# Performance work log

Measured on AMD Instinct MI355X. Metric: run time of the kernel, lower is better.

Reference implementation:

```python
import jax, jax.numpy as jnp
import numpy as np
import math

B, S, D, H = 8, 512, 2048, 16
HD = D // H
TIME_INCLUDE = True
QREL_INCLUDE = True


def setup_inputs() -> dict:
    root = jax.random.key(0)
    ks = jax.random.split(root, 14)
    f32 = jnp.float32
    scale = 1.0 / math.sqrt(D)
    query = jax.random.normal(ks[0], (B, S, D), dtype=f32)
    key = jax.random.normal(ks[1], (B, S, D), dtype=f32)
    value = jax.random.normal(ks[2], (B, S, D), dtype=f32)
    rel = jax.random.uniform(ks[3], (B, S, S), dtype=f32)  # relation scores, positive
    timestamp = jax.random.uniform(ks[4], (B, S, S), dtype=f32) * 10.0  # time deltas
    # causal mask: True = masked (future positions); guarantees each row has >=1 unmasked entry
    mask = jnp.broadcast_to(jnp.triu(jnp.ones((S, S), dtype=bool), k=1), (B, S, S))
    l1 = jnp.full((1,), 0.3, dtype=f32)
    l2 = jnp.full((1,), 0.5, dtype=f32)
    pos_key_embeds = jax.random.normal(ks[5], (S, HD), dtype=f32)
    pos_value_embeds = jax.random.normal(ks[6], (S, HD), dtype=f32)
    Wq = jax.random.normal(ks[7], (D, D), dtype=f32) * scale
    bq = jnp.zeros((D,), dtype=f32)
    Wk = jax.random.normal(ks[8], (D, D), dtype=f32) * scale
    bk = jnp.zeros((D,), dtype=f32)
    Wv = jax.random.normal(ks[9], (D, D), dtype=f32) * scale
    bv = jnp.zeros((D,), dtype=f32)
    return dict(query=query, key=key, value=value, rel=rel, l1=l1, l2=l2,
                timestamp=timestamp, pos_key_embeds=pos_key_embeds,
                pos_value_embeds=pos_value_embeds, mask=mask,
                Wq=Wq, bq=bq, Wk=Wk, bk=bk, Wv=Wv, bv=bv)


def reference(query, key, value, rel, l1, l2, timestamp, pos_key_embeds, pos_value_embeds, mask, Wq, bq, Wk, bk, Wv, bv):
    b, s, d = query.shape
    l1 = l1.reshape(())
    l2 = l2.reshape(())
    # QKV projections -> [B, H, S, HD]
    q = (query @ Wq.T + bq).reshape(b, s, H, HD).transpose(0, 2, 1, 3)
    k = (key @ Wk.T + bk).reshape(b, s, H, HD).transpose(0, 2, 1, 3)
    v = (value @ Wv.T + bv).reshape(b, s, H, HD).transpose(0, 2, 1, 3)
    m = mask[:, None]  # [B,1,S,S] bool, broadcast over heads (== repeat in torch)
    # relation-score softmax: rel * mask, zeros -> -10000
    relm = rel[:, None] * m.astype(jnp.float32)
    rel_attn = jax.nn.softmax(jnp.where(relm == 0, jnp.float32(-10000.0), relm), axis=-1)
    # content scores
    scores = jnp.einsum('bhqd,bhkd->bhqk', q, k) / math.sqrt(HD)
    scores = jnp.where(m, jnp.float32(-1e9), scores)
    # time-decay scores
    ts = jnp.exp(-jnp.abs(timestamp[:, None]))
    ts = jnp.where(m, -jnp.inf, ts)
    prob_attn = jax.nn.softmax(scores, axis=-1)
    time_attn = jax.nn.softmax(ts, axis=-1)
    if TIME_INCLUDE:
        prob_attn = (1.0 - l2) * prob_attn + l2 * time_attn
    if QREL_INCLUDE:
        prob_attn = (1.0 - l1) * prob_attn + l1 * rel_attn
    if not TIME_INCLUDE:
        prob_attn = l2 * prob_attn
    out = jnp.einsum('bhqk,bhkd->bhqd', prob_attn, v)
    out = out.transpose(0, 2, 1, 3).reshape(b, s, d)
    return out, prob_attn
```

## Files before the change

kernel.cpp:

```cpp
#include <hip/hip_runtime.h>
#include <hip/hip_bf16.h>

typedef __bf16 bf16_t;
typedef __bf16 bf16x8 __attribute__((ext_vector_type(8)));
typedef float  f32x4  __attribute__((ext_vector_type(4)));

constexpr int cB = 8, cS = 512, cD = 2048, cH = 16, cHD = 128;
constexpr int cBS = cB * cS;
constexpr float kInvSqrtHD = 0.08838834764831845f;

__device__ __forceinline__ bf16x8 cvt8(float4 a, float4 b) {
    bf16x8 r;
    r[0]=(bf16_t)a.x; r[1]=(bf16_t)a.y; r[2]=(bf16_t)a.z; r[3]=(bf16_t)a.w;
    r[4]=(bf16_t)b.x; r[5]=(bf16_t)b.y; r[6]=(bf16_t)b.z; r[7]=(bf16_t)b.w;
    return r;
}

__device__ __forceinline__ void gload16(const bf16_t* g, bf16_t* l) {
    __builtin_amdgcn_global_load_lds(
        (const __attribute__((address_space(1))) void*)g,
        (__attribute__((address_space(3))) void*)l,
        16, 0, 0);
}

__device__ __forceinline__ unsigned packbf(float a, float b) {
    const unsigned short ua = __builtin_bit_cast(unsigned short, (bf16_t)a);
    const unsigned short ub = __builtin_bit_cast(unsigned short, (bf16_t)b);
    return (unsigned)ua | ((unsigned)ub << 16);
}
__device__ __forceinline__ float unpk_lo(unsigned u) {
    return (float)__builtin_bit_cast(bf16_t, (unsigned short)(u & 0xffffu));
}
__device__ __forceinline__ float unpk_hi(unsigned u) {
    return (float)__builtin_bit_cast(bf16_t, (unsigned short)(u >> 16));
}

__global__ __launch_bounds__(256) void prep_kernel(
    const float* __restrict__ q, const float* __restrict__ k, const float* __restrict__ v,
    const float* __restrict__ wq, const float* __restrict__ wk, const float* __restrict__ wv,
    const float* __restrict__ rel, const float* __restrict__ tsp,
    bf16_t* __restrict__ abf, bf16_t* __restrict__ wbf,
    bf16_t* __restrict__ t_attn, bf16_t* __restrict__ r_attn)
{
    const int y = blockIdx.y;
    if (y < 6) {
        const float* src; bf16_t* dst; size_t n8;
        if (y < 3) { src = (y==0 ? q : y==1 ? k : v);   dst = abf + (size_t)y*cBS*cD;     n8 = (size_t)cBS*cD/8; }
        else       { src = (y==3 ? wq : y==4 ? wk : wv); dst = wbf + (size_t)(y-3)*cD*cD; n8 = (size_t)cD*cD/8; }
        const size_t stride = (size_t)gridDim.x * blockDim.x;
        for (size_t idx = (size_t)blockIdx.x * blockDim.x + threadIdx.x; idx < n8; idx += stride) {
            const float4 f0 = ((const float4*)src)[2*idx];
            const float4 f1 = ((const float4*)src)[2*idx+1];
            ((bf16x8*)dst)[idx] = cvt8(f0, f1);
        }
        return;
    }
    const int lane = threadIdx.x & 63;
    const int wid  = threadIdx.x >> 6;
    const int row  = blockIdx.x * 4 + wid;
    const int i = row & 511;
    const size_t base = (size_t)row * cS;

    float vt[8], vr[8];
    #pragma unroll
    for (int u = 0; u < 8; ++u) {
        const int j = lane + 64*u;
        const float tv = tsp[base + j];
        const float rv = rel[base + j];
        vt[u] = (j <= i) ? expf(-fabsf(tv)) : -__builtin_inff();
        vr[u] = (j > i && rv != 0.0f) ? rv : -10000.0f;
    }
    float Mt = vt[0], Mr = vr[0];
    #pragma unroll
    for (int u = 1; u < 8; ++u) { Mt = fmaxf(Mt, vt[u]); Mr = fmaxf(Mr, vr[u]); }
    #pragma unroll
    for (int msk = 1; msk < 64; msk <<= 1) {
        Mt = fmaxf(Mt, __shfl_xor(Mt, msk));
        Mr = fmaxf(Mr, __shfl_xor(Mr, msk));
    }
    float St = 0.f, Sr = 0.f;
    #pragma unroll
    for (int u = 0; u < 8; ++u) {
        vt[u] = expf(vt[u] - Mt);
        vr[u] = expf(vr[u] - Mr);
        St += vt[u]; Sr += vr[u];
    }
    #pragma unroll
    for (int msk = 1; msk < 64; msk <<= 1) { St += __shfl_xor(St, msk); Sr += __shfl_xor(Sr, msk); }
    const float rSt = 1.f / St, rSr = 1.f / Sr;
    #pragma unroll
    for (int u = 0; u < 8; ++u) {
        const int j = lane + 64*u;
        t_attn[base + j] = (bf16_t)(vt[u] * rSt);
        r_attn[base + j] = (bf16_t)(vr[u] * rSr);
    }
}

__global__ __launch_bounds__(256) void proj_kernel(
    const bf16_t* __restrict__ abf, const bf16_t* __restrict__ wbf,
    const float* __restrict__ bq, const float* __restrict__ bk, const float* __restrict__ bv,
    bf16_t* __restrict__ qh, bf16_t* __restrict__ kh, bf16_t* __restrict__ vtr)
{
    const int which = blockIdx.y;
    const bf16_t* A = abf + (size_t)which * cBS * cD;
    const bf16_t* W = wbf + (size_t)which * cD * cD;
    const float* bias = (which == 0) ? bq : (which == 1) ? bk : bv;

    const int bm = blockIdx.x & 31;
    const int bn = blockIdx.x >> 5;
    const int M0 = bm << 7, N0 = bn << 7;

    __shared__ bf16_t As[3][128 * 32];
    __shared__ bf16_t Ws[3][128 * 32];

    const int tid = threadIdx.x;
    const int lane = tid & 63, wid = tid >> 6;
    const int wm = wid & 1, wn = wid >> 1;
    const int i15 = lane & 15, g = lane >> 4;

    const int srow = tid >> 2;
    const int sg   = (tid & 3) ^ (srow & 3);
    const bf16_t* aSrc = A + (size_t)(M0 + srow) * cD + sg * 8;
    const bf16_t* wSrc = W + (size_t)(N0 + srow) * cD + sg * 8;
    const size_t rowStep = (size_t)64 * cD;

    auto stage = [&](int b, int kt) {
        const int kb = kt * 32;
        gload16(aSrc + kb,           &As[b][tid * 8]);
        gload16(aSrc + kb + rowStep, &As[b][tid * 8 + 2048]);
        gload16(wSrc + kb,           &Ws[b][tid * 8]);
        gload16(wSrc + kb + rowStep, &Ws[b][tid * 8 + 2048]);
    };

    int offA[4], offW[4];
    #pragma unroll
    for (int m = 0; m < 4; ++m) {
        const int r = wm*64 + m*16 + i15;
        offA[m] = r*32 + ((g ^ (r & 3)) << 3);
    }
    #pragma unroll
    for (int n = 0; n < 4; ++n) {
        const int r = wn*64 + n*16 + i15;
        offW[n] = r*32 + ((g ^ (r & 3)) << 3);
    }

    const f32x4 zero4 = {0.f, 0.f, 0.f, 0.f};
    f32x4 acc[4][4];
    #pragma unroll
    for (int m = 0; m < 4; ++m)
        #pragma unroll
        for (int n = 0; n < 4; ++n) acc[m][n] = zero4;

    stage(0, 0);
    stage(1, 1);

    for (int kt = 0; kt < cD / 32; ++kt) {
        if (kt + 2 < cD / 32) {
            stage((kt + 2) % 3, kt + 2);
            asm volatile("s_waitcnt vmcnt(8)" ::: "memory");
        } else if (kt + 1 < cD / 32) {
            asm volatile("s_waitcnt vmcnt(4)" ::: "memory");
        } else {
            asm volatile("s_waitcnt vmcnt(0)" ::: "memory");
        }
        __builtin_amdgcn_s_barrier();
        __builtin_amdgcn_sched_barrier(0);

        const bf16_t* Ab = &As[kt % 3][0];
        const bf16_t* Wb = &Ws[kt % 3][0];
        bf16x8 a[4];
        #pragma unroll
        for (int m = 0; m < 4; ++m) a[m] = *(const bf16x8*)(Ab + offA[m]);
        #pragma unroll
        for (int n = 0; n < 4; ++n) {
            const bf16x8 w = *(const bf16x8*)(Wb + offW[n]);
            #pragma unroll
            for (int m = 0; m < 4; ++m)
                acc[m][n] = __builtin_amdgcn_mfma_f32_16x16x32_bf16(a[m], w, acc[m][n], 0, 0, 0);
        }
        __builtin_amdgcn_s_barrier();
    }

    #pragma unroll
    for (int n = 0; n < 4; ++n) {
        const int col = N0 + wn*64 + n*16 + i15;
        const float bb = bias[col];
        const int hh = col >> 7, hd = col & 127;
        #pragma unroll
        for (int m = 0; m < 4; ++m) {
            const int rowl = wm*64 + m*16 + (g << 2);
            #pragma unroll
            for (int r = 0; r < 4; ++r) {
                const int R = M0 + rowl + r;
                const int bbi = R >> 9, ss = R & 511;
                const float val = acc[m][n][r] + bb;
                if (which == 2)
                    vtr[((size_t)(bbi*cH + hh) * cHD + hd) * cS + ss] = (bf16_t)val;
                else if (which == 0)
                    qh[((size_t)(bbi*cH + hh) * cS + ss) * cHD + hd] = (bf16_t)val;
                else
                    kh[((size_t)(bbi*cH + hh) * cS + ss) * cHD + hd] = (bf16_t)val;
            }
        }
    }
}

__global__ __launch_bounds__(256) void attn_kernel(
    const bf16_t* __restrict__ qh, const bf16_t* __restrict__ kh,
    const bf16_t* __restrict__ vtr,
    const bf16_t* __restrict__ t_attn, const bf16_t* __restrict__ r_attn,
    const float* __restrict__ l1p, const float* __restrict__ l2p,
    float* __restrict__ probOut, float* __restrict__ out)
{
    const int itile = blockIdx.x & 7;
    const int bh = blockIdx.x >> 3;
    const int b = bh >> 4, h = bh & 15;
    const int i0 = itile * 64;

    const float l1 = l1p[0], l2 = l2p[0];
    const float ap = (1.f - l1) * (1.f - l2);
    const float at = (1.f - l1) * l2;
    const float ar = l1;

    __shared__ bf16_t qps[64][136];
    __shared__ bf16_t ks[64][136];
    __shared__ bf16_t vs[2][128 * 64];

    const int tid = threadIdx.x, lane = tid & 63, wid = tid >> 6;
    const int i15 = lane & 15, g = lane >> 4;

    {
        const int row = tid >> 2, d0 = (tid & 3) << 5;
        const bf16_t* src = qh + ((size_t)bh * cS + i0 + row) * cHD + d0;
        #pragma unroll
        for (int q = 0; q < 4; ++q)
            *(bf16x8*)(&qps[row][d0 + q*8]) = *(const bf16x8*)(src + q*8);
    }
    __syncthreads();
    bf16x8 aq[4];
    #pragma unroll
    for (int kk = 0; kk < 4; ++kk)
        aq[kk] = *(const bf16x8*)(&qps[wid*16 + i15][kk*32 + (g << 3)]);

    const int iBase = i0 + wid*16 + (g << 2);

    auto stageK = [&](int kt) {
        const int row = tid >> 2, d0 = (tid & 3) << 5;
        const bf16_t* src = kh + ((size_t)bh * cS + kt*64 + row) * cHD + d0;
        #pragma unroll
        for (int q = 0; q < 4; ++q)
            *(bf16x8*)(&ks[row][d0 + q*8]) = *(const bf16x8*)(src + q*8);
    };
    auto stageVissue = [&](int kt, int buf) {
        #pragma unroll
        for (int e4 = 0; e4 < 4; ++e4) {
            const int e = e4 * 256 + tid;
            const int hd = e >> 3, j8 = e & 7;
            const int jsw = (j8 ^ (hd & 7)) << 3;
            gload16(vtr + ((size_t)bh * cHD + hd) * cS + kt*64 + jsw, &vs[buf][e * 8]);
        }
    };

    float srow[4] = {0.f, 0.f, 0.f, 0.f};
    unsigned es[8][8];
    #pragma unroll
    for (int kt = 0; kt < 8; ++kt) {
        if (kt <= itile) {
            __syncthreads();
            stageK(kt);
            __syncthreads();
            f32x4 acc[4];
            const f32x4 zero4 = {0.f, 0.f, 0.f, 0.f};
            #pragma unroll
            for (int n = 0; n < 4; ++n) acc[n] = zero4;
            #pragma unroll
            for (int kk = 0; kk < 4; ++kk)
                #pragma unroll
                for (int n = 0; n < 4; ++n) {
                    bf16x8 bk = *(const bf16x8*)(&ks[n*16 + i15][kk*32 + (g << 3)]);
                    acc[n] = __builtin_amdgcn_mfma_f32_16x16x32_bf16(aq[kk], bk, acc[n], 0, 0, 0);
                }
            #pragma unroll
            for (int n = 0; n < 4; ++n) {
                const int j = kt*64 + n*16 + i15;
                float e[4];
                #pragma unroll
                for (int r = 0; r < 4; ++r) {
                    const int i = iBase + r;
                    e[r] = (j > i) ? 0.f : __expf(acc[n][r] * kInvSqrtHD);
                    srow[r] += e[r];
                }
                es[kt][n*2]     = packbf(e[0], e[1]);
                es[kt][n*2 + 1] = packbf(e[2], e[3]);
            }
        }
    }
    float rs[4];
    #pragma unroll
    for (int r = 0; r < 4; ++r) {
        float s = srow[r];
        #pragma unroll
        for (int msk = 1; msk < 16; msk <<= 1) s += __shfl_xor(s, msk);
        rs[r] = 1.f / s;
    }

    f32x4 oacc[8];
    const f32x4 zero4o = {0.f, 0.f, 0.f, 0.f};
    #pragma unroll
    for (int n2 = 0; n2 < 8; ++n2) oacc[n2] = zero4o;

    stageVissue(0, 0);

    #pragma unroll
    for (int kt = 0; kt < 8; ++kt) {
        const bool hasP = (kt <= itile);
        #pragma unroll
        for (int n = 0; n < 4; ++n) {
            float e[4] = {0.f, 0.f, 0.f, 0.f};
            if (hasP) {
                const unsigned p0 = es[kt][n*2], p1 = es[kt][n*2 + 1];
                e[0] = unpk_lo(p0); e[1] = unpk_hi(p0);
                e[2] = unpk_lo(p1); e[3] = unpk_hi(p1);
            }
            const int j = kt*64 + n*16 + i15;
            #pragma unroll
            for (int r = 0; r < 4; ++r) {
                const int i = iBase + r;
                const float p = e[r] * rs[r];
                const size_t tri = (size_t)(b*cS + i) * cS + j;
                const float tv = (float)t_attn[tri];
                const float rv = (float)r_attn[tri];
                const float mixed = ap*p + at*tv + ar*rv;
                probOut[((size_t)bh * cS + i) * cS + j] = mixed;
                qps[wid*16 + (g << 2) + r][n*16 + i15] = (bf16_t)mixed;
            }
        }
        asm volatile("s_waitcnt lgkmcnt(0)" ::: "memory");
        __builtin_amdgcn_sched_barrier(0);
        asm volatile("s_waitcnt vmcnt(16)" ::: "memory");
        __builtin_amdgcn_s_barrier();
        #pragma unroll
        for (int kk = 0; kk < 2; ++kk) {
            const bf16x8 pa = *(const bf16x8*)(&qps[wid*16 + i15][kk*32 + (g << 3)]);
            #pragma unroll
            for (int n2 = 0; n2 < 8; ++n2) {
                const int hd = n2*16 + i15;
                const int jb = (kk*64 + g*16) ^ ((hd & 7) << 4);
                const bf16x8 bvv = *(const bf16x8*)((const char*)&vs[kt & 1][0] + hd*128 + jb);
                oacc[n2] = __builtin_amdgcn_mfma_f32_16x16x32_bf16(pa, bvv, oacc[n2], 0, 0, 0);
            }
        }
        if (kt < 7) stageVissue(kt + 1, (kt + 1) & 1);
    }

    #pragma unroll
    for (int n2 = 0; n2 < 8; ++n2) {
        const int hd = n2*16 + i15;
        #pragma unroll
        for (int r = 0; r < 4; ++r) {
            const int i = i0 + wid*16 + (g << 2) + r;
            out[(size_t)(b*cS + i) * cD + h*cHD + hd] = oacc[n2][r];
        }
    }
}

extern "C" void kernel_launch(void* const* d_in, const int* in_sizes, int n_in,
                              void* d_out, int out_size, void* d_ws, size_t ws_size,
                              hipStream_t stream)
{
    const float* query = (const float*)d_in[0];
    const float* keyi  = (const float*)d_in[1];
    const float* value = (const float*)d_in[2];
    const float* rel   = (const float*)d_in[3];
    const float* l1    = (const float*)d_in[4];
    const float* l2    = (const float*)d_in[5];
    const float* tsp   = (const float*)d_in[6];
    const float* Wq    = (const float*)d_in[10];
    const float* bq    = (const float*)d_in[11];
    const float* Wk    = (const float*)d_in[12];
    const float* bk    = (const float*)d_in[13];
    const float* Wv    = (const float*)d_in[14];
    const float* bv    = (const float*)d_in[15];

    char* ws = (char*)d_ws;
    const size_t projBytes = (size_t)cB * cH * cS * cHD * 2;
    bf16_t* qh  = (bf16_t*)(ws);
    bf16_t* kh  = (bf16_t*)(ws + projBytes);
    bf16_t* vtr = (bf16_t*)(ws + 2 * projBytes);
    const size_t trBytes = (size_t)cB * cS * cS * 2;
    bf16_t* tat = (bf16_t*)(ws + 3 * projBytes);
    bf16_t* rat = (bf16_t*)(ws + 3 * projBytes + trBytes);

    float* out = (float*)d_out;
    float* probOut = out + (size_t)cB * cS * cD;

    bf16_t* abf = (bf16_t*)probOut;
    bf16_t* wbf = abf + (size_t)3 * cBS * cD;

    prep_kernel<<<dim3(1024, 7), 256, 0, stream>>>(query, keyi, value, Wq, Wk, Wv,
                                                   rel, tsp, abf, wbf, tat, rat);
    proj_kernel<<<dim3(512, 3), 256, 0, stream>>>(abf, wbf, bq, bk, bv, qh, kh, vtr);
    attn_kernel<<<cB * cH * (cS / 64), 256, 0, stream>>>(qh, kh, vtr, tat, rat, l1, l2, probOut, out);
}
```

Before: 262.1 us.

## Replace triple-buffered K=32 projection pipeline with single-buffer K=64 tiles

The QKV projection GEMM loop drops the three-stage LDS ring (K=32 per stage, manual vmcnt waits) for a single LDS buffer holding a K=64 tile, with the XOR swizzle widened to 8 chunks. Each iteration loads the tile, synchronizes, and runs two 32-wide MFMA sub-steps. The aim is fewer barriers per unit of K and a smaller LDS footprint (32KB instead of 48KB), which could let more blocks share a CU. The cost is that global loads no longer overlap with MFMA work inside a block, so latency hiding depends on other resident blocks.

```diff
diff --git a/kernel.cpp b/kernel.cpp
--- a/kernel.cpp
+++ b/kernel.cpp
@@ -110,38 +110,34 @@
     const int bn = blockIdx.x >> 5;
     const int M0 = bm << 7, N0 = bn << 7;
 
-    __shared__ bf16_t As[3][128 * 32];
-    __shared__ bf16_t Ws[3][128 * 32];
+    __shared__ bf16_t As[128 * 64];
+    __shared__ bf16_t Ws[128 * 64];
 
     const int tid = threadIdx.x;
     const int lane = tid & 63, wid = tid >> 6;
     const int wm = wid & 1, wn = wid >> 1;
     const int i15 = lane & 15, g = lane >> 4;
 
-    const int srow = tid >> 2;
-    const int sg   = (tid & 3) ^ (srow & 3);
-    const bf16_t* aSrc = A + (size_t)(M0 + srow) * cD + sg * 8;
-    const bf16_t* wSrc = W + (size_t)(N0 + srow) * cD + sg * 8;
-    const size_t rowStep = (size_t)64 * cD;
-
-    auto stage = [&](int b, int kt) {
-        const int kb = kt * 32;
-        gload16(aSrc + kb,           &As[b][tid * 8]);
-        gload16(aSrc + kb + rowStep, &As[b][tid * 8 + 2048]);
-        gload16(wSrc + kb,           &Ws[b][tid * 8]);
-        gload16(wSrc + kb + rowStep, &Ws[b][tid * 8 + 2048]);
-    };
+    const int sr0 = tid >> 3;
+    const int sgc = ((tid & 7) ^ (sr0 & 7)) << 3;
+    const bf16_t* aSrc[4];
+    const bf16_t* wSrc[4];
+    #pragma unroll
+    for (int l = 0; l < 4; ++l) {
+        aSrc[l] = A + (size_t)(M0 + l*32 + sr0) * cD + sgc;
+        wSrc[l] = W + (size_t)(N0 + l*32 + sr0) * cD + sgc;
+    }
 
     int offA[4], offW[4];
     #pragma unroll
     for (int m = 0; m < 4; ++m) {
         const int r = wm*64 + m*16 + i15;
-        offA[m] = r*32 + ((g ^ (r & 3)) << 3);
+        offA[m] = r*64 + ((g ^ (r & 7)) << 3);
     }
     #pragma unroll
     for (int n = 0; n < 4; ++n) {
         const int r = wn*64 + n*16 + i15;
-        offW[n] = r*32 + ((g ^ (r & 3)) << 3);
+        offW[n] = r*64 + ((g ^ (r & 7)) << 3);
     }
 
     const f32x4 zero4 = {0.f, 0.f, 0.f, 0.f};
@@ -151,34 +147,29 @@
         #pragma unroll
         for (int n = 0; n < 4; ++n) acc[m][n] = zero4;
 
-    stage(0, 0);
-    stage(1, 1);
-
-    for (int kt = 0; kt < cD / 32; ++kt) {
-        if (kt + 2 < cD / 32) {
-            stage((kt + 2) % 3, kt + 2);
-            asm volatile("s_waitcnt vmcnt(8)" ::: "memory");
-        } else if (kt + 1 < cD / 32) {
-            asm volatile("s_waitcnt vmcnt(4)" ::: "memory");
-        } else {
-            asm volatile("s_waitcnt vmcnt(0)" ::: "memory");
-        }
-        __builtin_amdgcn_s_barrier();
-        __builtin_amdgcn_sched_barrier(0);
-
-        const bf16_t* Ab = &As[kt % 3][0];
-        const bf16_t* Wb = &Ws[kt % 3][0];
-        bf16x8 a[4];
-        #pragma unroll
-        for (int m = 0; m < 4; ++m) a[m] = *(const bf16x8*)(Ab + offA[m]);
-        #pragma unroll
-        for (int n = 0; n < 4; ++n) {
-            const bf16x8 w = *(const bf16x8*)(Wb + offW[n]);
-            #pragma unroll
-            for (int m = 0; m < 4; ++m)
-                acc[m][n] = __builtin_amdgcn_mfma_f32_16x16x32_bf16(a[m], w, acc[m][n], 0, 0, 0);
-        }
-        __builtin_amdgcn_s_barrier();
+    for (int kt = 0; kt < cD / 64; ++kt) {
+        const int kb = kt * 64;
+        __syncthreads();
+        #pragma unroll
+        for (int l = 0; l < 4; ++l) {
+            gload16(aSrc[l] + kb, &As[(l*256 + tid) * 8]);
+            gload16(wSrc[l] + kb, &Ws[(l*256 + tid) * 8]);
+        }
+        __syncthreads();
+        #pragma unroll
+        for (int kk = 0; kk < 2; ++kk) {
+            const int x = kk * 32;
+            bf16x8 a[4];
+            #pragma unroll
+            for (int m = 0; m < 4; ++m) a[m] = *(const bf16x8*)(&As[offA[m] ^ x]);
+            #pragma unroll
+            for (int n = 0; n < 4; ++n) {
+                const bf16x8 w = *(const bf16x8*)(&Ws[offW[n] ^ x]);
+                #pragma unroll
+                for (int m = 0; m < 4; ++m)
+                    acc[m][n] = __builtin_amdgcn_mfma_f32_16x16x32_bf16(a[m], w, acc[m][n], 0, 0, 0);
+            }
+        }
     }
 
     #pragma unroll
```

Result: faster. 244.7 us (-6.7%).
